# Performance work log

Hardware: AMD Instinct MI355X
Metric: run time of the kernel (lower is better)

The kernel has to match this reference:

```python
import jax, jax.numpy as jnp
import numpy as np

N_NODES = 50000
N_EDGES = 800000
IN_DIM = 128
HIDDEN = 64
HEADS = 4
OUT_DIM = 32
NEG_SLOPE = 0.2  # PyG GATConv default negative_slope


def _glorot(key, shape):
    fan = shape[0] + shape[-1]
    return jax.random.normal(key, shape, dtype=jnp.float32) * jnp.sqrt(2.0 / fan)


def setup_inputs() -> dict:
    key = jax.random.key(0)
    ks = jax.random.split(key, 8)
    x = jax.random.normal(ks[0], (N_NODES, IN_DIM), dtype=jnp.float32)
    edge_index = jax.random.randint(ks[1], (2, N_EDGES), 0, N_NODES, dtype=jnp.int64)
    return {
        "x": x,
        "edge_index": edge_index,
        "W1": _glorot(ks[2], (IN_DIM, HEADS * HIDDEN)),
        "a_src1": _glorot(ks[3], (HEADS, HIDDEN)),
        "a_dst1": _glorot(ks[4], (HEADS, HIDDEN)),
        "b1": jnp.zeros((HEADS * HIDDEN,), dtype=jnp.float32),
        "W2": _glorot(ks[5], (HEADS * HIDDEN, OUT_DIM)),
        "a_src2": _glorot(ks[6], (1, OUT_DIM)),
        "a_dst2": _glorot(ks[7], (1, OUT_DIM)),
        "b2": jnp.zeros((OUT_DIM,), dtype=jnp.float32),
    }


def gat_conv(x, src, dst, W, a_src, a_dst, b, heads, feat, concat):
    """PyG-style GATConv (self-loops already appended to src/dst)."""
    n = x.shape[0]
    h = (x @ W).reshape(n, heads, feat)              # [N, H, F]
    alpha_s = jnp.einsum("nhf,hf->nh", h, a_src)     # [N, H]
    alpha_d = jnp.einsum("nhf,hf->nh", h, a_dst)     # [N, H]
    logits = jax.nn.leaky_relu(alpha_s[src] + alpha_d[dst], NEG_SLOPE)  # [E, H]
    # segment softmax over edges grouped by destination node
    seg_max = jax.ops.segment_max(logits, dst, num_segments=n)          # [N, H]
    expd = jnp.exp(logits - seg_max[dst])
    seg_sum = jax.ops.segment_sum(expd, dst, num_segments=n)            # [N, H]
    alpha = expd / (seg_sum[dst] + 1e-16)                               # [E, H]
    # scatter-aggregate weighted messages from source nodes
    out = jax.ops.segment_sum(h[src] * alpha[:, :, None], dst, num_segments=n)  # [N, H, F]
    out = out.reshape(n, heads * feat) if concat else out.mean(axis=1)
    return out + b


def reference(x, edge_index, W1, a_src1, a_dst1, b1, W2, a_src2, a_dst2, b2):
    n = x.shape[0]
    loop = jnp.arange(n, dtype=edge_index.dtype)
    src = jnp.concatenate([edge_index[0], loop])  # add_self_loops=True (PyG default)
    dst = jnp.concatenate([edge_index[1], loop])
    h = jax.nn.elu(gat_conv(x, src, dst, W1, a_src1, a_dst1, b1, HEADS, HIDDEN, True))
    return gat_conv(h, src, dst, W2, a_src2, a_dst2, b2, 1, OUT_DIM, False)
```

## Files before the change

### kernel.cpp

```cpp
#include <hip/hip_runtime.h>
#include <hip/hip_bf16.h>

#define N_NODES 50000
#define N_EDGES 800000
#define E_TOT   850000
#define IN_DIM  128
#define C1      256
#define HEADS   4
#define HID     64
#define OUT_DIM 32
#define NEG_SLOPE 0.2f
#define SCAN_NBLK 196

typedef __attribute__((ext_vector_type(8))) short bf16x8;
typedef __attribute__((ext_vector_type(8))) unsigned short u16x8;
typedef __attribute__((ext_vector_type(4))) float f32x4;

__device__ __forceinline__ void edge_sd(const int* __restrict__ ei, int e, int& s, int& d) {
    if (e < N_EDGES) { s = ei[e]; d = ei[N_EDGES + e]; }
    else             { s = d = e - N_EDGES; }
}

__device__ __forceinline__ unsigned short f2bf(float f) {
    unsigned u = __float_as_uint(f);
    u += 0x7fffu + ((u >> 16) & 1u);
    return (unsigned short)(u >> 16);
}
__device__ __forceinline__ float bf2f(unsigned short u) {
    return __uint_as_float(((unsigned)u) << 16);
}

__global__ __launch_bounds__(256) void deg_kernel(const int* __restrict__ ei,
                                                  int* __restrict__ deg) {
    int e = blockIdx.x * 256 + threadIdx.x;
    if (e >= E_TOT) return;
    int s, d; edge_sd(ei, e, s, d);
    atomicAdd(&deg[d], 1);
}

__global__ __launch_bounds__(256) void scanA_kernel(const int* __restrict__ deg,
                                                    int* __restrict__ incl,
                                                    int* __restrict__ blocksum) {
    __shared__ int sm[256];
    int t = threadIdx.x, idx = blockIdx.x * 256 + t;
    int v = (idx < N_NODES) ? deg[idx] : 0;
    sm[t] = v; __syncthreads();
#pragma unroll
    for (int off = 1; off < 256; off <<= 1) {
        int u = (t >= off) ? sm[t - off] : 0;
        __syncthreads();
        sm[t] += u;
        __syncthreads();
    }
    if (idx < N_NODES) incl[idx] = sm[t];
    if (t == 255) blocksum[blockIdx.x] = sm[t];
}

__global__ __launch_bounds__(256) void scanC_kernel(const int* __restrict__ deg,
                                                    const int* __restrict__ incl,
                                                    const int* __restrict__ blocksum,
                                                    int* __restrict__ row_start) {
    __shared__ int wsum[4];
    int t = threadIdx.x;
    int v = (t < (int)blockIdx.x) ? blocksum[t] : 0;
#pragma unroll
    for (int m = 32; m >= 1; m >>= 1) v += __shfl_xor(v, m, 64);
    if ((t & 63) == 0) wsum[t >> 6] = v;
    __syncthreads();
    int off = wsum[0] + wsum[1] + wsum[2] + wsum[3];
    int idx = blockIdx.x * 256 + t;
    if (idx >= N_NODES) return;
    row_start[idx] = off + incl[idx] - deg[idx];
    if (idx == N_NODES - 1) row_start[N_NODES] = off + incl[idx];
}

__global__ __launch_bounds__(256) void scatter_kernel(const int* __restrict__ ei,
                                                      const int* __restrict__ row_start,
                                                      int* __restrict__ cursor,
                                                      int* __restrict__ csr_src) {
    int e = blockIdx.x * 256 + threadIdx.x;
    if (e >= E_TOT) return;
    int s, d; edge_sd(ei, e, s, d);
    int pos = atomicAdd(&cursor[d], 1);
    csr_src[row_start[d] + pos] = s;
}

__global__ __launch_bounds__(256) void setup_kernel(const float* __restrict__ W1,
                                                    const float* __restrict__ W2,
                                                    unsigned short* __restrict__ Bp1,
                                                    unsigned short* __restrict__ Bp2) {
    int tid = blockIdx.x * 256 + threadIdx.x;
    if (tid < IN_DIM * C1) {
        int j = tid & 7, q = (tid >> 3) & 3, n = (tid >> 5) & 255, K0 = tid >> 13;
        int k = K0 * 32 + q * 8 + j;
        Bp1[tid] = f2bf(W1[k * C1 + n]);
    } else if (tid < IN_DIM * C1 + C1 * OUT_DIM) {
        int t2 = tid - IN_DIM * C1;
        int j = t2 & 7, q = (t2 >> 3) & 3, n = (t2 >> 5) & 31, K0 = t2 >> 10;
        int k = K0 * 32 + q * 8 + j;
        Bp2[t2] = f2bf(W2[k * OUT_DIM + n]);
    }
}

__global__ __launch_bounds__(256) void gemm1_kernel(const float* __restrict__ x,
                                                    const unsigned short* __restrict__ Bp,
                                                    const float* __restrict__ a_src1,
                                                    const float* __restrict__ a_dst1,
                                                    unsigned short* __restrict__ h1b,
                                                    float* __restrict__ as1,
                                                    float* __restrict__ ad1) {
    __shared__ unsigned short xs[16][136];
    const int t = threadIdx.x;
    const int row0 = blockIdx.x * 16;
    {
        int r = t >> 4, k0 = (t & 15) * 8;
        const float* xp = &x[(size_t)(row0 + r) * IN_DIM + k0];
        float4 v0 = *(const float4*)xp;
        float4 v1 = *(const float4*)(xp + 4);
        ushort4 o0, o1;
        o0.x = f2bf(v0.x); o0.y = f2bf(v0.y); o0.z = f2bf(v0.z); o0.w = f2bf(v0.w);
        o1.x = f2bf(v1.x); o1.y = f2bf(v1.y); o1.z = f2bf(v1.z); o1.w = f2bf(v1.w);
        *(ushort4*)&xs[r][k0] = o0;
        *(ushort4*)&xs[r][k0 + 4] = o1;
    }
    __syncthreads();
    const int wave = t >> 6;
    const int lane = t & 63;
    const int nl = lane & 15, q = lane >> 4;
    f32x4 acc[4];
    f32x4 z = {0.f, 0.f, 0.f, 0.f};
    acc[0] = z; acc[1] = z; acc[2] = z; acc[3] = z;
#pragma unroll
    for (int K0 = 0; K0 < 4; ++K0) {
        bf16x8 af = *(const bf16x8*)&xs[nl][K0 * 32 + q * 8];
#pragma unroll
        for (int sub = 0; sub < 4; ++sub) {
            int n = wave * 64 + sub * 16 + nl;
            bf16x8 bfv = *(const bf16x8*)&Bp[((size_t)(K0 * 256 + n) * 4 + q) * 8];
            acc[sub] = __builtin_amdgcn_mfma_f32_16x16x32_bf16(af, bfv, acc[sub], 0, 0, 0);
        }
    }
    float asv[4], adv[4];
#pragma unroll
    for (int sub = 0; sub < 4; ++sub) {
        asv[sub] = a_src1[wave * 64 + sub * 16 + nl];
        adv[sub] = a_dst1[wave * 64 + sub * 16 + nl];
    }
#pragma unroll
    for (int r = 0; r < 4; ++r) {
        int gr = row0 + q * 4 + r;
        float ps = 0.f, pd = 0.f;
#pragma unroll
        for (int sub = 0; sub < 4; ++sub) {
            float v = acc[sub][r];
            h1b[(size_t)gr * C1 + wave * 64 + sub * 16 + nl] = f2bf(v);
            ps += v * asv[sub];
            pd += v * adv[sub];
        }
#pragma unroll
        for (int m = 8; m >= 1; m >>= 1) {
            ps += __shfl_xor(ps, m, 16);
            pd += __shfl_xor(pd, m, 16);
        }
        if (nl == 0) {
            as1[gr * 4 + wave] = ps;
            ad1[gr * 4 + wave] = pd;
        }
    }
}

__global__ __launch_bounds__(256) void agg1_kernel(const int* __restrict__ csr_src,
                                                   const int* __restrict__ row_start,
                                                   const unsigned short* __restrict__ h1b,
                                                   const float* __restrict__ as1,
                                                   const float* __restrict__ ad1,
                                                   const float* __restrict__ b1,
                                                   unsigned short* __restrict__ hpb) {
    int n = (blockIdx.x * 256 + threadIdx.x) >> 6;
    if (n >= N_NODES) return;
    int lane = threadIdx.x & 63;
    int e2 = lane >> 5;
    int c  = lane & 31;
    int h  = c >> 3;
    int beg = row_start[n], end = row_start[n + 1];
    float ad = ad1[n * 4 + h];
    float acc[8] = {0.f, 0.f, 0.f, 0.f, 0.f, 0.f, 0.f, 0.f};
    float sumw = 0.f;
    for (int i = beg; i < end; i += 8) {
#pragma unroll
        for (int u = 0; u < 4; ++u) {
            int idx = i + e2 + 2 * u;
            bool valid = idx < end;
            int ic = valid ? idx : beg;
            int s = csr_src[ic];
            float l = as1[s * 4 + h] + ad;
            l = l > 0.f ? l : NEG_SLOPE * l;
            float w = valid ? __expf(l) : 0.f;
            sumw += w;
            u16x8 rv = *(const u16x8*)&h1b[(size_t)s * C1 + c * 8];
#pragma unroll
            for (int k = 0; k < 8; ++k) acc[k] += w * bf2f(rv[k]);
        }
    }
    sumw += __shfl_xor(sumw, 32, 64);
#pragma unroll
    for (int k = 0; k < 8; ++k) acc[k] += __shfl_xor(acc[k], 32, 64);
    if (e2 == 0) {
        float inv = 1.f / (sumw + 1e-16f);
        const float4 b0 = *(const float4*)&b1[c * 8];
        const float4 b4 = *(const float4*)&b1[c * 8 + 4];
        float bb[8] = {b0.x, b0.y, b0.z, b0.w, b4.x, b4.y, b4.z, b4.w};
        u16x8 o;
#pragma unroll
        for (int k = 0; k < 8; ++k) {
            float v = acc[k] * inv + bb[k];
            v = v > 0.f ? v : __expf(v) - 1.f;
            o[k] = f2bf(v);
        }
        *(u16x8*)&hpb[(size_t)n * C1 + c * 8] = o;
    }
}

__global__ __launch_bounds__(256) void gemm2_kernel(const unsigned short* __restrict__ hpb,
                                                    const unsigned short* __restrict__ Bp2,
                                                    const float* __restrict__ a_src2,
                                                    const float* __restrict__ a_dst2,
                                                    float* __restrict__ h2,
                                                    float* __restrict__ as2,
                                                    float* __restrict__ ad2) {
    __shared__ unsigned short xs[64][264];
    const int t = threadIdx.x;
    const int row0 = blockIdx.x * 64;
    for (int idx = t; idx < 2048; idx += 256) {
        int r = idx >> 5, ch = (idx & 31) * 8;
        int gr = row0 + r;
        u16x8 v = {0, 0, 0, 0, 0, 0, 0, 0};
        if (gr < N_NODES) v = *(const u16x8*)&hpb[(size_t)gr * C1 + ch];
        *(u16x8*)&xs[r][ch] = v;
    }
    __syncthreads();
    const int wave = t >> 6, lane = t & 63;
    const int nl = lane & 15, q = lane >> 4;
    f32x4 acc0 = {0.f, 0.f, 0.f, 0.f}, acc1 = {0.f, 0.f, 0.f, 0.f};
#pragma unroll
    for (int K0 = 0; K0 < 8; ++K0) {
        bf16x8 af = *(const bf16x8*)&xs[wave * 16 + nl][K0 * 32 + q * 8];
        bf16x8 b0 = *(const bf16x8*)&Bp2[((size_t)(K0 * 32 + nl) * 4 + q) * 8];
        bf16x8 b1v = *(const bf16x8*)&Bp2[((size_t)(K0 * 32 + 16 + nl) * 4 + q) * 8];
        acc0 = __builtin_amdgcn_mfma_f32_16x16x32_bf16(af, b0, acc0, 0, 0, 0);
        acc1 = __builtin_amdgcn_mfma_f32_16x16x32_bf16(af, b1v, acc1, 0, 0, 0);
    }
    float a_s0 = a_src2[nl], a_s1 = a_src2[16 + nl];
    float a_d0 = a_dst2[nl], a_d1 = a_dst2[16 + nl];
#pragma unroll
    for (int r = 0; r < 4; ++r) {
        int gr = row0 + wave * 16 + q * 4 + r;
        if (gr < N_NODES) {
            h2[(size_t)gr * OUT_DIM + nl] = acc0[r];
            h2[(size_t)gr * OUT_DIM + 16 + nl] = acc1[r];
            float ps = acc0[r] * a_s0 + acc1[r] * a_s1;
            float pd = acc0[r] * a_d0 + acc1[r] * a_d1;
#pragma unroll
            for (int m = 8; m >= 1; m >>= 1) {
                ps += __shfl_xor(ps, m, 16);
                pd += __shfl_xor(pd, m, 16);
            }
            if (nl == 0) { as2[gr] = ps; ad2[gr] = pd; }
        }
    }
}

__global__ __launch_bounds__(256) void agg2_kernel(const int* __restrict__ csr_src,
                                                   const int* __restrict__ row_start,
                                                   const float* __restrict__ h2,
                                                   const float* __restrict__ as2,
                                                   const float* __restrict__ ad2,
                                                   const float* __restrict__ b2,
                                                   float* __restrict__ out) {
    int n = (blockIdx.x * 256 + threadIdx.x) >> 6;
    if (n >= N_NODES) return;
    int lane = threadIdx.x & 63;
    int g  = lane >> 3;
    int c4 = lane & 7;
    int beg = row_start[n], end = row_start[n + 1];
    float ad = ad2[n];
    float4 acc = make_float4(0.f, 0.f, 0.f, 0.f);
    float sumw = 0.f;
    for (int i = beg; i < end; i += 8) {
        int idx = i + g;
        bool valid = idx < end;
        int ic = valid ? idx : beg;
        int s = csr_src[ic];
        float l = as2[s] + ad;
        l = l > 0.f ? l : NEG_SLOPE * l;
        float w = valid ? __expf(l) : 0.f;
        sumw += w;
        float4 hv = *(const float4*)&h2[(size_t)s * OUT_DIM + c4 * 4];
        acc.x += w * hv.x; acc.y += w * hv.y; acc.z += w * hv.z; acc.w += w * hv.w;
    }
#pragma unroll
    for (int m = 8; m <= 32; m <<= 1) {
        sumw  += __shfl_xor(sumw, m, 64);
        acc.x += __shfl_xor(acc.x, m, 64);
        acc.y += __shfl_xor(acc.y, m, 64);
        acc.z += __shfl_xor(acc.z, m, 64);
        acc.w += __shfl_xor(acc.w, m, 64);
    }
    if (g == 0) {
        float inv = 1.f / (sumw + 1e-16f);
        const float4 bv = *(const float4*)&b2[c4 * 4];
        *(float4*)&out[(size_t)n * OUT_DIM + c4 * 4] =
            make_float4(acc.x * inv + bv.x, acc.y * inv + bv.y,
                        acc.z * inv + bv.z, acc.w * inv + bv.w);
    }
}

extern "C" void kernel_launch(void* const* d_in, const int* in_sizes, int n_in,
                              void* d_out, int out_size, void* d_ws, size_t ws_size,
                              hipStream_t stream) {
    const float* x      = (const float*)d_in[0];
    const int*   ei     = (const int*)d_in[1];
    const float* W1     = (const float*)d_in[2];
    const float* a_src1 = (const float*)d_in[3];
    const float* a_dst1 = (const float*)d_in[4];
    const float* b1     = (const float*)d_in[5];
    const float* W2     = (const float*)d_in[6];
    const float* a_src2 = (const float*)d_in[7];
    const float* a_dst2 = (const float*)d_in[8];
    const float* b2     = (const float*)d_in[9];
    float* out = (float*)d_out;

    unsigned short* h1b = (unsigned short*)d_ws;
    unsigned short* hpb = h1b + 12800000;
    unsigned short* Bp1 = hpb + 12800000;
    unsigned short* Bp2 = Bp1 + 32768;
    float* h2     = (float*)(Bp2 + 8192);
    float* as1    = h2 + 1600000;
    float* ad1    = as1 + 200000;
    float* as2    = ad1 + 200000;
    float* ad2    = as2 + 50000;
    int* csr_src  = (int*)(ad2 + 50000);
    int* row_start= csr_src + E_TOT;
    int* deg      = row_start + (N_NODES + 1);
    int* cursor   = deg + N_NODES;
    int* incl     = cursor + N_NODES;
    int* blocksum = incl + N_NODES;

    hipMemsetAsync(deg, 0, (size_t)(2 * N_NODES) * 4, stream);

    const int EB = (E_TOT + 255) / 256;
    setup_kernel<<<160, 256, 0, stream>>>(W1, W2, Bp1, Bp2);
    deg_kernel<<<EB, 256, 0, stream>>>(ei, deg);
    scanA_kernel<<<SCAN_NBLK, 256, 0, stream>>>(deg, incl, blocksum);
    scanC_kernel<<<SCAN_NBLK, 256, 0, stream>>>(deg, incl, blocksum, row_start);
    scatter_kernel<<<EB, 256, 0, stream>>>(ei, row_start, cursor, csr_src);

    gemm1_kernel<<<N_NODES / 16, 256, 0, stream>>>(x, Bp1, a_src1, a_dst1, h1b, as1, ad1);
    agg1_kernel<<<(N_NODES * 64 + 255) / 256, 256, 0, stream>>>(csr_src, row_start, h1b, as1, ad1, b1, hpb);

    gemm2_kernel<<<(N_NODES + 63) / 64, 256, 0, stream>>>(hpb, Bp2, a_src2, a_dst2, h2, as2, ad2);
    agg2_kernel<<<(N_NODES * 64 + 255) / 256, 256, 0, stream>>>(csr_src, row_start, h2, as2, ad2, b2, out);
}
```

Measured before the change: 311.9 us.

## Restructure layer-1 aggregation, store layer-2 features as bf16, fold memset into setup

The layer-1 aggregation now gives each lane 4 contiguous channels of one edge. It batches 8 source indices, gathers and attention loads per iteration to raise memory-level parallelism, and drops the cross-half shuffle reduction. Layer-2 node features are written and gathered as bf16 instead of fp32, which halves the gather traffic in agg2 at some precision cost. The degree and cursor memset moves into the weight-packing setup kernel, removing one API call.

Measured after the change: 302.9 us. 1.03x faster.

```diff
diff --git a/kernel.cpp b/kernel.cpp
--- a/kernel.cpp
+++ b/kernel.cpp
@@ -29,6 +29,28 @@
 __device__ __forceinline__ float bf2f(unsigned short u) {
     return __uint_as_float(((unsigned)u) << 16);
 }
+__device__ __forceinline__ float4 bf4_to_f4(ushort4 v) {
+    return make_float4(bf2f(v.x), bf2f(v.y), bf2f(v.z), bf2f(v.w));
+}
+
+__global__ __launch_bounds__(256) void setup_kernel(const float* __restrict__ W1,
+                                                    const float* __restrict__ W2,
+                                                    unsigned short* __restrict__ Bp1,
+                                                    unsigned short* __restrict__ Bp2,
+                                                    int* __restrict__ degcur) {
+    int tid = blockIdx.x * 256 + threadIdx.x;
+    if (tid < 2 * N_NODES) degcur[tid] = 0;
+    if (tid < IN_DIM * C1) {
+        int j = tid & 7, q = (tid >> 3) & 3, n = (tid >> 5) & 255, K0 = tid >> 13;
+        int k = K0 * 32 + q * 8 + j;
+        Bp1[tid] = f2bf(W1[k * C1 + n]);
+        if (tid < C1 * OUT_DIM) {
+            int j2 = tid & 7, q2 = (tid >> 3) & 3, n2 = (tid >> 5) & 31, K02 = tid >> 10;
+            int k2 = K02 * 32 + q2 * 8 + j2;
+            Bp2[tid] = f2bf(W2[k2 * OUT_DIM + n2]);
+        }
+    }
+}
 
 __global__ __launch_bounds__(256) void deg_kernel(const int* __restrict__ ei,
                                                   int* __restrict__ deg) {
@@ -83,23 +105,6 @@
     int s, d; edge_sd(ei, e, s, d);
     int pos = atomicAdd(&cursor[d], 1);
     csr_src[row_start[d] + pos] = s;
-}
-
-__global__ __launch_bounds__(256) void setup_kernel(const float* __restrict__ W1,
-                                                    const float* __restrict__ W2,
-                                                    unsigned short* __restrict__ Bp1,
-                                                    unsigned short* __restrict__ Bp2) {
-    int tid = blockIdx.x * 256 + threadIdx.x;
-    if (tid < IN_DIM * C1) {
-        int j = tid & 7, q = (tid >> 3) & 3, n = (tid >> 5) & 255, K0 = tid >> 13;
-        int k = K0 * 32 + q * 8 + j;
-        Bp1[tid] = f2bf(W1[k * C1 + n]);
-    } else if (tid < IN_DIM * C1 + C1 * OUT_DIM) {
-        int t2 = tid - IN_DIM * C1;
-        int j = t2 & 7, q = (t2 >> 3) & 3, n = (t2 >> 5) & 31, K0 = t2 >> 10;
-        int k = K0 * 32 + q * 8 + j;
-        Bp2[t2] = f2bf(W2[k * OUT_DIM + n]);
-    }
 }
 
 __global__ __launch_bounds__(256) void gemm1_kernel(const float* __restrict__ x,
@@ -179,53 +184,75 @@
     int n = (blockIdx.x * 256 + threadIdx.x) >> 6;
     if (n >= N_NODES) return;
     int lane = threadIdx.x & 63;
-    int e2 = lane >> 5;
-    int c  = lane & 31;
-    int h  = c >> 3;
+    int h = lane >> 4;
     int beg = row_start[n], end = row_start[n + 1];
     float ad = ad1[n * 4 + h];
-    float acc[8] = {0.f, 0.f, 0.f, 0.f, 0.f, 0.f, 0.f, 0.f};
+    float4 acc = make_float4(0.f, 0.f, 0.f, 0.f);
     float sumw = 0.f;
-    for (int i = beg; i < end; i += 8) {
-#pragma unroll
-        for (int u = 0; u < 4; ++u) {
-            int idx = i + e2 + 2 * u;
-            bool valid = idx < end;
-            int ic = valid ? idx : beg;
-            int s = csr_src[ic];
-            float l = as1[s * 4 + h] + ad;
+    int i = beg;
+    for (; i + 8 <= end; i += 8) {
+        int s[8];
+#pragma unroll
+        for (int u = 0; u < 8; ++u) s[u] = csr_src[i + u];
+        ushort4 rv[8];
+#pragma unroll
+        for (int u = 0; u < 8; ++u) rv[u] = *(const ushort4*)&h1b[(size_t)s[u] * C1 + lane * 4];
+        float a[8];
+#pragma unroll
+        for (int u = 0; u < 8; ++u) a[u] = as1[s[u] * 4 + h];
+#pragma unroll
+        for (int u = 0; u < 8; ++u) {
+            float l = a[u] + ad;
             l = l > 0.f ? l : NEG_SLOPE * l;
-            float w = valid ? __expf(l) : 0.f;
+            float w = __expf(l);
             sumw += w;
-            u16x8 rv = *(const u16x8*)&h1b[(size_t)s * C1 + c * 8];
-#pragma unroll
-            for (int k = 0; k < 8; ++k) acc[k] += w * bf2f(rv[k]);
-        }
-    }
-    sumw += __shfl_xor(sumw, 32, 64);
-#pragma unroll
-    for (int k = 0; k < 8; ++k) acc[k] += __shfl_xor(acc[k], 32, 64);
-    if (e2 == 0) {
-        float inv = 1.f / (sumw + 1e-16f);
-        const float4 b0 = *(const float4*)&b1[c * 8];
-        const float4 b4 = *(const float4*)&b1[c * 8 + 4];
-        float bb[8] = {b0.x, b0.y, b0.z, b0.w, b4.x, b4.y, b4.z, b4.w};
-        u16x8 o;
-#pragma unroll
-        for (int k = 0; k < 8; ++k) {
-            float v = acc[k] * inv + bb[k];
-            v = v > 0.f ? v : __expf(v) - 1.f;
-            o[k] = f2bf(v);
-        }
-        *(u16x8*)&hpb[(size_t)n * C1 + c * 8] = o;
-    }
+            float4 f = bf4_to_f4(rv[u]);
+            acc.x += w * f.x; acc.y += w * f.y; acc.z += w * f.z; acc.w += w * f.w;
+        }
+    }
+    if (i < end) {
+        int s[8]; bool va[8];
+#pragma unroll
+        for (int u = 0; u < 8; ++u) {
+            va[u] = (i + u) < end;
+            s[u] = csr_src[va[u] ? i + u : beg];
+        }
+        ushort4 rv[8];
+#pragma unroll
+        for (int u = 0; u < 8; ++u) rv[u] = *(const ushort4*)&h1b[(size_t)s[u] * C1 + lane * 4];
+        float a[8];
+#pragma unroll
+        for (int u = 0; u < 8; ++u) a[u] = as1[s[u] * 4 + h];
+#pragma unroll
+        for (int u = 0; u < 8; ++u) {
+            float l = a[u] + ad;
+            l = l > 0.f ? l : NEG_SLOPE * l;
+            float w = va[u] ? __expf(l) : 0.f;
+            sumw += w;
+            float4 f = bf4_to_f4(rv[u]);
+            acc.x += w * f.x; acc.y += w * f.y; acc.z += w * f.z; acc.w += w * f.w;
+        }
+    }
+    float inv = 1.f / (sumw + 1e-16f);
+    const float4 bv = *(const float4*)&b1[lane * 4];
+    float v0 = acc.x * inv + bv.x;
+    float v1 = acc.y * inv + bv.y;
+    float v2 = acc.z * inv + bv.z;
+    float v3 = acc.w * inv + bv.w;
+    v0 = v0 > 0.f ? v0 : __expf(v0) - 1.f;
+    v1 = v1 > 0.f ? v1 : __expf(v1) - 1.f;
+    v2 = v2 > 0.f ? v2 : __expf(v2) - 1.f;
+    v3 = v3 > 0.f ? v3 : __expf(v3) - 1.f;
+    ushort4 o;
+    o.x = f2bf(v0); o.y = f2bf(v1); o.z = f2bf(v2); o.w = f2bf(v3);
+    *(ushort4*)&hpb[(size_t)n * C1 + lane * 4] = o;
 }
 
 __global__ __launch_bounds__(256) void gemm2_kernel(const unsigned short* __restrict__ hpb,
                                                     const unsigned short* __restrict__ Bp2,
                                                     const float* __restrict__ a_src2,
                                                     const float* __restrict__ a_dst2,
-                                                    float* __restrict__ h2,
+                                                    unsigned short* __restrict__ h2b,
                                                     float* __restrict__ as2,
                                                     float* __restrict__ ad2) {
     __shared__ unsigned short xs[64][264];
@@ -256,8 +283,8 @@
     for (int r = 0; r < 4; ++r) {
         int gr = row0 + wave * 16 + q * 4 + r;
         if (gr < N_NODES) {
-            h2[(size_t)gr * OUT_DIM + nl] = acc0[r];
-            h2[(size_t)gr * OUT_DIM + 16 + nl] = acc1[r];
+            h2b[(size_t)gr * OUT_DIM + nl] = f2bf(acc0[r]);
+            h2b[(size_t)gr * OUT_DIM + 16 + nl] = f2bf(acc1[r]);
             float ps = acc0[r] * a_s0 + acc1[r] * a_s1;
             float pd = acc0[r] * a_d0 + acc1[r] * a_d1;
 #pragma unroll
@@ -272,7 +299,7 @@
 
 __global__ __launch_bounds__(256) void agg2_kernel(const int* __restrict__ csr_src,
                                                    const int* __restrict__ row_start,
-                                                   const float* __restrict__ h2,
+                                                   const unsigned short* __restrict__ h2b,
                                                    const float* __restrict__ as2,
                                                    const float* __restrict__ ad2,
                                                    const float* __restrict__ b2,
@@ -295,7 +322,7 @@
         l = l > 0.f ? l : NEG_SLOPE * l;
         float w = valid ? __expf(l) : 0.f;
         sumw += w;
-        float4 hv = *(const float4*)&h2[(size_t)s * OUT_DIM + c4 * 4];
+        float4 hv = bf4_to_f4(*(const ushort4*)&h2b[(size_t)s * OUT_DIM + c4 * 4]);
         acc.x += w * hv.x; acc.y += w * hv.y; acc.z += w * hv.z; acc.w += w * hv.w;
     }
 #pragma unroll
@@ -332,10 +359,10 @@
 
     unsigned short* h1b = (unsigned short*)d_ws;
     unsigned short* hpb = h1b + 12800000;
-    unsigned short* Bp1 = hpb + 12800000;
+    unsigned short* h2b = hpb + 12800000;
+    unsigned short* Bp1 = h2b + 1600000;
     unsigned short* Bp2 = Bp1 + 32768;
-    float* h2     = (float*)(Bp2 + 8192);
-    float* as1    = h2 + 1600000;
+    float* as1    = (float*)(Bp2 + 8192);
     float* ad1    = as1 + 200000;
     float* as2    = ad1 + 200000;
     float* ad2    = as2 + 50000;
@@ -346,10 +373,8 @@
     int* incl     = cursor + N_NODES;
     int* blocksum = incl + N_NODES;
 
-    hipMemsetAsync(deg, 0, (size_t)(2 * N_NODES) * 4, stream);
-
     const int EB = (E_TOT + 255) / 256;
-    setup_kernel<<<160, 256, 0, stream>>>(W1, W2, Bp1, Bp2);
+    setup_kernel<<<391, 256, 0, stream>>>(W1, W2, Bp1, Bp2, deg);
     deg_kernel<<<EB, 256, 0, stream>>>(ei, deg);
     scanA_kernel<<<SCAN_NBLK, 256, 0, stream>>>(deg, incl, blocksum);
     scanC_kernel<<<SCAN_NBLK, 256, 0, stream>>>(deg, incl, blocksum, row_start);
@@ -358,6 +383,6 @@
     gemm1_kernel<<<N_NODES / 16, 256, 0, stream>>>(x, Bp1, a_src1, a_dst1, h1b, as1, ad1);
     agg1_kernel<<<(N_NODES * 64 + 255) / 256, 256, 0, stream>>>(csr_src, row_start, h1b, as1, ad1, b1, hpb);
 
-    gemm2_kernel<<<(N_NODES + 63) / 64, 256, 0, stream>>>(hpb, Bp2, a_src2, a_dst2, h2, as2, ad2);
-    agg2_kernel<<<(N_NODES * 64 + 255) / 256, 256, 0, stream>>>(csr_src, row_start, h2, as2, ad2, b2, out);
-}
+    gemm2_kernel<<<(N_NODES + 63) / 64, 256, 0, stream>>>(hpb, Bp2, a_src2, a_dst2, h2b, as2, ad2);
+    agg2_kernel<<<(N_NODES * 64 + 255) / 256, 256, 0, stream>>>(csr_src, row_start, h2b, as2, ad2, b2, out);
+}
```
